# Performance work log

Hardware: AMD Instinct MI355X
Metric: run time of the kernel (lower is better)

Reference implementation:

```python
import jax, jax.numpy as jnp
import numpy as np

KERNEL_EPS = 1e-4  # performer-pytorch softmax_kernel eps


def _softmax_kernel(data, projection, is_query):
    # data: [b, h, n, d]; projection: [m, d]
    d = data.shape[-1]
    m = projection.shape[0]
    data_normalizer = d ** -0.25
    ratio = m ** -0.5
    # random-feature logits: [b, h, n, m]
    data_dash = jnp.einsum('bhnd,md->bhnm', data * data_normalizer, projection)
    # ||x||^2 / 2 * normalizer^2, [b, h, n, 1]
    diag = 0.5 * (data_normalizer ** 2) * jnp.sum(data * data, axis=-1, keepdims=True)
    if is_query:
        stab = jnp.max(data_dash, axis=-1, keepdims=True)
    else:
        stab = jnp.max(data_dash)  # global max, as in performer-pytorch
    return ratio * (jnp.exp(data_dash - diag - stab) + KERNEL_EPS)


def _linear_attention(q, k, v):
    # q, k: [b, h, n, m] random features; v: [b, h, n, e]
    k_cumsum = jnp.sum(k, axis=-2)                                   # [b, h, m]
    d_inv = 1.0 / jnp.einsum('bhnm,bhm->bhn', q, k_cumsum)           # [b, h, n]
    context = jnp.einsum('bhnm,bhne->bhme', k, v)                    # [b, h, m, e]
    return jnp.einsum('bhme,bhnm,bhn->bhne', context, q, d_inv)      # [b, h, n, e]


def setup_inputs() -> dict:
    key = jax.random.key(0)
    kq, kk, kv = jax.random.split(key, 3)
    b, h, n, d = 8, 16, 4096, 64
    nb_features = 256
    query = jax.random.normal(kq, (b, h, n, d), dtype=jnp.float32)
    key_t = jax.random.normal(kk, (b, h, n, d), dtype=jnp.float32)
    value = jax.random.normal(kv, (b, h, n, d), dtype=jnp.float32)
    # Gaussian orthogonal random matrix (performer-pytorch, scaling=0):
    # stack of d x d orthonormal blocks, rows rescaled to chi(d) norms.
    rng = np.random.RandomState(0)
    blocks = []
    for _ in range(nb_features // d + 1):
        qmat, _ = np.linalg.qr(rng.randn(d, d))
        blocks.append(qmat.T)
    proj = np.concatenate(blocks, axis=0)[:nb_features]
    multiplier = np.linalg.norm(rng.randn(nb_features, d), axis=1)
    projection = jnp.asarray(multiplier[:, None] * proj, dtype=jnp.float32)
    return {"query": query, "key": key_t, "value": value, "projection": projection}


def reference(query, key, value, projection):
    q_prime = _softmax_kernel(query, projection, is_query=True)   # [b,h,n,m]
    k_prime = _softmax_kernel(key, projection, is_query=False)    # [b,h,n,m]
    return _linear_attention(q_prime, k_prime, value)             # [b,h,n,e]
```

## Files before the change

kernel.cpp:

```cpp
#include <hip/hip_runtime.h>
#include <hip/hip_bf16.h>

typedef __attribute__((ext_vector_type(4))) float f32x4;
typedef __attribute__((ext_vector_type(8))) short short8;
typedef __attribute__((ext_vector_type(4))) unsigned short us4;
typedef __attribute__((ext_vector_type(4))) unsigned int u32x4;

#define BH_ 128
#define N_ 4096
#define LOG2E 1.4426950408889634f
#define NORML (0.35355339059327373f * LOG2E)
#define DIAGL (0.0625f * LOG2E)
#define EPSF 1e-4f

#if __has_builtin(__builtin_amdgcn_exp2f)
#define EXP2F(x) __builtin_amdgcn_exp2f(x)
#else
#define EXP2F(x) exp2f(x)
#endif

#define BARRIER_LGKM() asm volatile("s_waitcnt lgkmcnt(0)\ns_barrier" ::: "memory")

static __device__ __forceinline__ unsigned short f2bf(float f) {
  return __bfloat16_as_ushort(__float2bfloat16(f));
}
static __device__ __forceinline__ float bf2f(unsigned short s) {
  return __uint_as_float(((unsigned int)s) << 16);
}
static __device__ __forceinline__ us4 cvt4(f32x4 x) {
  us4 r;
  r[0] = f2bf(x[0]); r[1] = f2bf(x[1]); r[2] = f2bf(x[2]); r[3] = f2bf(x[3]);
  return r;
}
static __device__ __forceinline__ unsigned int pk2bf(float lo, float hi) {
  unsigned int r;
  asm("v_cvt_pk_bf16_f32 %0, %1, %2" : "=v"(r) : "v"(lo), "v"(hi));
  return r;
}

static __device__ __forceinline__ int posm(int m) {
  return (m & 0xE0) | ((m & 0xC) << 1) | ((m & 0x10) >> 2) | (m & 3);
}

__global__ void perf_prep(const float* __restrict__ proj,
                          unsigned short* __restrict__ projb) {
  int i = blockIdx.x * 256 + threadIdx.x;
  projb[i] = f2bf(proj[i] * NORML);
}

__global__ __launch_bounds__(256, 2)
void perf_kpass(const float* __restrict__ kp, const float* __restrict__ vp,
                const float* __restrict__ proj, float* __restrict__ ctxp,
                float* __restrict__ kexpp, float* __restrict__ vsump,
                unsigned int* __restrict__ gmaxb, int nchunk) {
  const int bh = blockIdx.x & (BH_ - 1);
  const int chunk = blockIdx.x >> 7;
  const int chunkrows = N_ / nchunk;
  const int tiles = chunkrows >> 5;
  const int t = threadIdx.x;
  const int wid = t >> 6;
  const int lane = t & 63;
  const int g = lane >> 4;
  const int c = lane & 15;

  __shared__ __align__(16) unsigned short sX[2][32][72];
  __shared__ __align__(16) unsigned short sVt[2][64][40];
  __shared__ float sDiag[2][32];
  __shared__ float sVsum[64];
  __shared__ float sGm[4];

  short8 pfrag[4][2];
#pragma unroll
  for (int mt = 0; mt < 4; ++mt)
#pragma unroll
    for (int kk = 0; kk < 2; ++kk) {
      const float* src = proj + (wid * 64 + mt * 16 + c) * 64 + kk * 32 + g * 8;
      short8 v;
#pragma unroll
      for (int j = 0; j < 8; ++j) v[j] = (short)f2bf(src[j] * NORML);
      pfrag[mt][kk] = v;
    }

  f32x4 ctx[4][4];
#pragma unroll
  for (int i = 0; i < 4; ++i)
#pragma unroll
    for (int j = 0; j < 4; ++j) ctx[i][j] = (f32x4){0.f, 0.f, 0.f, 0.f};

  float kexpreg[4] = {0.f, 0.f, 0.f, 0.f};
  float vsum0 = 0.f, vsum1 = 0.f, vsum2 = 0.f, vsum3 = 0.f;
  float gm = -1e30f;

  const float* kb0 = kp + ((size_t)bh * N_ + (size_t)chunk * chunkrows) * 64;
  const float* vb0 = vp + ((size_t)bh * N_ + (size_t)chunk * chunkrows) * 64;

  f32x4 kx[2], vx[2];
#pragma unroll
  for (int hh = 0; hh < 2; ++hh) {
    int f = t + hh * 256;
    kx[hh] = *(const f32x4*)(kb0 + (f >> 4) * 64 + (f & 15) * 4);
    vx[hh] = *(const f32x4*)(vb0 + (f >> 4) * 64 + (f & 15) * 4);
  }

  for (int nt = 0; nt < tiles; ++nt) {
    const int buf = nt & 1;
#pragma unroll
    for (int hh = 0; hh < 2; ++hh) {
      int f = t + hh * 256;
      int row = f >> 4;
      int c4 = f & 15;
      f32x4 x = kx[hh];
      float ss = x[0] * x[0] + x[1] * x[1] + x[2] * x[2] + x[3] * x[3];
      ss += __shfl_xor(ss, 1);
      ss += __shfl_xor(ss, 2);
      ss += __shfl_xor(ss, 4);
      ss += __shfl_xor(ss, 8);
      if (c4 == 0) sDiag[buf][row] = DIAGL * ss;
      *(us4*)&sX[buf][row][c4 * 4] = cvt4(x);
      f32x4 vv = vx[hh];
      vsum0 += vv[0]; vsum1 += vv[1]; vsum2 += vv[2]; vsum3 += vv[3];
      const int ks = ((row >> 2) & 3) * 8 + (row >> 4) * 4 + (row & 3);
#pragma unroll
      for (int jj = 0; jj < 4; ++jj) {
        int j = (jj + t) & 3;
        float val = (j == 0) ? vv[0] : (j == 1) ? vv[1] : (j == 2) ? vv[2] : vv[3];
        sVt[buf][c4 * 4 + j][ks] = f2bf(val);
      }
    }
    if (nt + 1 < tiles) {
      const float* kb = kb0 + (nt + 1) * 2048;
      const float* vb = vb0 + (nt + 1) * 2048;
#pragma unroll
      for (int hh = 0; hh < 2; ++hh) {
        int f = t + hh * 256;
        kx[hh] = *(const f32x4*)(kb + (f >> 4) * 64 + (f & 15) * 4);
        vx[hh] = *(const f32x4*)(vb + (f >> 4) * 64 + (f & 15) * 4);
      }
    }
    BARRIER_LGKM();

    short8 afr[2][2];
#pragma unroll
    for (int nh1 = 0; nh1 < 2; ++nh1)
#pragma unroll
      for (int kk = 0; kk < 2; ++kk)
        afr[nh1][kk] = *(const short8*)&sX[buf][nh1 * 16 + c][kk * 32 + g * 8];

    f32x4 acc1[2][4];
#pragma unroll
    for (int i = 0; i < 2; ++i)
#pragma unroll
      for (int j = 0; j < 4; ++j) acc1[i][j] = (f32x4){0.f, 0.f, 0.f, 0.f};
#pragma unroll
    for (int kk = 0; kk < 2; ++kk)
#pragma unroll
      for (int nh1 = 0; nh1 < 2; ++nh1)
#pragma unroll
        for (int mt = 0; mt < 4; ++mt)
          acc1[nh1][mt] = __builtin_amdgcn_mfma_f32_16x16x32_bf16(
              afr[nh1][kk], pfrag[mt][kk], acc1[nh1][mt], 0, 0, 0);

    short8 wfrag[4];
#pragma unroll
    for (int mt = 0; mt < 4; ++mt) {
#pragma unroll
      for (int nh1 = 0; nh1 < 2; ++nh1)
#pragma unroll
        for (int r = 0; r < 4; ++r) {
          float dd = acc1[nh1][mt][r];
          gm = fmaxf(gm, dd);
          int n = nh1 * 16 + g * 4 + r;
          float w = EXP2F(dd - sDiag[buf][n]);
          unsigned short wb = f2bf(w);
          kexpreg[mt] += bf2f(wb);
          wfrag[mt][nh1 * 4 + r] = (short)wb;
        }
    }

    short8 bvv[4];
#pragma unroll
    for (int et = 0; et < 4; ++et)
      bvv[et] = *(const short8*)&sVt[buf][et * 16 + c][g * 8];
#pragma unroll
    for (int mt2 = 0; mt2 < 4; ++mt2)
#pragma unroll
      for (int et = 0; et < 4; ++et)
        ctx[mt2][et] = __builtin_amdgcn_mfma_f32_16x16x32_bf16(
            wfrag[mt2], bvv[et], ctx[mt2][et], 0, 0, 0);
  }

#pragma unroll
  for (int mt2 = 0; mt2 < 4; ++mt2)
#pragma unroll
    for (int et = 0; et < 4; ++et) {
      int m0 = wid * 64 + mt2 * 16 + g * 4;
      int e = et * 16 + c;
      size_t base = (((size_t)chunk * BH_ + bh) * 64 + e) * 256 + m0;
      *(f32x4*)(ctxp + base) = ctx[mt2][et];
    }
#pragma unroll
  for (int mt = 0; mt < 4; ++mt) {
    float s = kexpreg[mt];
    s += __shfl_xor(s, 16);
    s += __shfl_xor(s, 32);
    if (lane < 16)
      kexpp[((size_t)chunk * BH_ + bh) * 256 + wid * 64 + mt * 16 + lane] = s;
  }
  if (t < 64) sVsum[t] = 0.f;
  __syncthreads();
  atomicAdd(&sVsum[(t & 15) * 4 + 0], vsum0);
  atomicAdd(&sVsum[(t & 15) * 4 + 1], vsum1);
  atomicAdd(&sVsum[(t & 15) * 4 + 2], vsum2);
  atomicAdd(&sVsum[(t & 15) * 4 + 3], vsum3);
  __syncthreads();
  if (t < 64) vsump[((size_t)chunk * BH_ + bh) * 64 + t] = sVsum[t];

  gm = fmaxf(gm, __shfl_xor(gm, 1));
  gm = fmaxf(gm, __shfl_xor(gm, 2));
  gm = fmaxf(gm, __shfl_xor(gm, 4));
  gm = fmaxf(gm, __shfl_xor(gm, 8));
  gm = fmaxf(gm, __shfl_xor(gm, 16));
  gm = fmaxf(gm, __shfl_xor(gm, 32));
  if (lane == 0) sGm[wid] = gm;
  __syncthreads();
  if (t == 0) {
    float mm = fmaxf(fmaxf(sGm[0], sGm[1]), fmaxf(sGm[2], sGm[3]));
    atomicMax((int*)gmaxb, __float_as_int(mm));
  }
}

__global__ void perf_rescale(const float* __restrict__ ctxp,
                             const float* __restrict__ kexpp,
                             const float* __restrict__ vsump,
                             unsigned short* __restrict__ ctxt,
                             unsigned short* __restrict__ kchi,
                             unsigned short* __restrict__ kclo,
                             const unsigned int* __restrict__ gmaxb, int nchunk) {
  const int bh = blockIdx.x >> 3;
  const int es = blockIdx.x & 7;
  const int t = threadIdx.x;
  const int pos = posm(t);
  const float gmax = __uint_as_float(*gmaxb);
  const float s = EXP2F(-gmax);
  if (es == 0) {
    float acc = 0.f;
    for (int cc = 0; cc < nchunk; ++cc)
      acc += kexpp[((size_t)cc * BH_ + bh) * 256 + t];
    float kcv = s * acc + EPSF * (float)N_;
    unsigned short hi = f2bf(kcv);
    kchi[bh * 256 + pos] = hi;
    kclo[bh * 256 + pos] = f2bf(kcv - bf2f(hi));
  }
  for (int e = es * 8; e < es * 8 + 8; ++e) {
    float vs = 0.f;
    for (int cc = 0; cc < nchunk; ++cc)
      vs += vsump[((size_t)cc * BH_ + bh) * 64 + e];
    float a2 = 0.f;
    for (int cc = 0; cc < nchunk; ++cc)
      a2 += ctxp[(((size_t)cc * BH_ + bh) * 64 + e) * 256 + t];
    ctxt[((size_t)bh * 64 + e) * 256 + pos] = f2bf(s * a2 + EPSF * vs);
  }
}

__global__ __launch_bounds__(256, 2)
void perf_qpass(const float* __restrict__ qp,
                const unsigned short* __restrict__ projb,
                const unsigned short* __restrict__ ctxt,
                const unsigned short* __restrict__ kchi,
                const unsigned short* __restrict__ kclo,
                float* __restrict__ outp) {
  const int bh = blockIdx.x >> 3;
  const int chunk = blockIdx.x & 7;
  const int t = threadIdx.x;
  const int wid = t >> 6;
  const int lane = t & 63;
  const int g = lane >> 4;
  const int c = lane & 15;

  __shared__ __align__(16) unsigned short sP[256 * 64];
  __shared__ __align__(16) unsigned short sC[64 * 256];
  __shared__ __align__(16) unsigned short sC2[16 * 256];

  const unsigned short* csrc = ctxt + (size_t)bh * 64 * 256;
  const unsigned short* khib = kchi + bh * 256;
  const unsigned short* klob = kclo + bh * 256;

  const float* qbase = qp + ((size_t)bh * N_ + chunk * 512 + wid * 128) * 64;
  float* obase = outp + ((size_t)bh * N_ + chunk * 512 + wid * 128) * 64;

  const float* q0 = qbase + (size_t)c * 64 + g * 8;
  f32x4 xp0 = *(const f32x4*)(q0);
  f32x4 xp1 = *(const f32x4*)(q0 + 4);
  f32x4 xp2 = *(const f32x4*)(q0 + 32);
  f32x4 xp3 = *(const f32x4*)(q0 + 36);

#pragma unroll
  for (int rep = 0; rep < 8; ++rep) {
    int e = rep * 2048 + t * 8;
    {
      int row = e >> 6, slot = (e & 63) >> 3;
      short8 v = *(const short8*)(projb + e);
      *(short8*)((char*)sP + row * 128 + ((slot ^ (row & 7)) << 4)) = v;
    }
    {
      int row = e >> 8, slot = (e & 255) >> 3;
      short8 v = *(const short8*)(csrc + e);
      *(short8*)((char*)sC + row * 512 + ((slot ^ (row & 7)) << 4)) = v;
    }
  }
#pragma unroll
  for (int rep = 0; rep < 2; ++rep) {
    int e = rep * 2048 + t * 8;
    int row = e >> 8, col = e & 255, slot = col >> 3;
    short8 v = {0, 0, 0, 0, 0, 0, 0, 0};
    if (row == 0) v = *(const short8*)(khib + col);
    if (row == 1) v = *(const short8*)(klob + col);
    *(short8*)((char*)sC2 + row * 512 + ((slot ^ (row & 7)) << 4)) = v;
  }
  __syncthreads();

  const int gsw = (g ^ (c & 3)) << 4;
  const int b6 = (c >> 2) & 1;
  const int pb0 = c * 128 + (b6 << 6) + gsw;
  const int pb1 = c * 128 + ((1 ^ b6) << 6) + gsw;
  const char* spc = (const char*)sP;
  const char* scc = (const char*)sC + c * 512;
  const char* sc2c = (const char*)sC2 + c * 512;

#pragma unroll 1
  for (int tt = 0; tt < 8; ++tt) {
    f32x4 x0 = xp0, x1 = xp1, x2 = xp2, x3 = xp3;
    if (tt + 1 < 8) {
      const float* qn = qbase + ((size_t)((tt + 1) * 16 + c)) * 64 + g * 8;
      xp0 = *(const f32x4*)(qn);
      xp1 = *(const f32x4*)(qn + 4);
      xp2 = *(const f32x4*)(qn + 32);
      xp3 = *(const f32x4*)(qn + 36);
    }
    float ss = x0[0]*x0[0] + x0[1]*x0[1] + x0[2]*x0[2] + x0[3]*x0[3]
             + x1[0]*x1[0] + x1[1]*x1[1] + x1[2]*x1[2] + x1[3]*x1[3]
             + x2[0]*x2[0] + x2[1]*x2[1] + x2[2]*x2[2] + x2[3]*x2[3]
             + x3[0]*x3[0] + x3[1]*x3[1] + x3[2]*x3[2] + x3[3]*x3[3];
    ss += __shfl_xor(ss, 16);
    ss += __shfl_xor(ss, 32);
    const float diag = DIAGL * ss;

    short8 xb0, xb1;
#pragma unroll
    for (int j = 0; j < 4; ++j) {
      xb0[j] = (short)f2bf(x0[j]);
      xb0[j + 4] = (short)f2bf(x1[j]);
      xb1[j] = (short)f2bf(x2[j]);
      xb1[j + 4] = (short)f2bf(x3[j]);
    }

    f32x4 acc1[16];
#pragma unroll
    for (int mt = 0; mt < 16; ++mt) acc1[mt] = (f32x4){0.f, 0.f, 0.f, 0.f};
    short8 Ak0[4], Ak1[4], Bk0[4], Bk1[4];
#pragma unroll
    for (int i = 0; i < 4; ++i) {
      Ak0[i] = *(const short8*)(spc + i * 2048 + pb0);
      Ak1[i] = *(const short8*)(spc + i * 2048 + pb1);
    }
#pragma unroll
    for (int i = 0; i < 4; ++i) {
      Bk0[i] = *(const short8*)(spc + (4 + i) * 2048 + pb0);
      Bk1[i] = *(const short8*)(spc + (4 + i) * 2048 + pb1);
    }
#pragma unroll
    for (int i = 0; i < 4; ++i) {
      acc1[i] = __builtin_amdgcn_mfma_f32_16x16x32_bf16(Ak0[i], xb0, acc1[i], 0, 0, 0);
      acc1[i] = __builtin_amdgcn_mfma_f32_16x16x32_bf16(Ak1[i], xb1, acc1[i], 0, 0, 0);
    }
#pragma unroll
    for (int i = 0; i < 4; ++i) {
      Ak0[i] = *(const short8*)(spc + (8 + i) * 2048 + pb0);
      Ak1[i] = *(const short8*)(spc + (8 + i) * 2048 + pb1);
    }
#pragma unroll
    for (int i = 0; i < 4; ++i) {
      acc1[4 + i] = __builtin_amdgcn_mfma_f32_16x16x32_bf16(Bk0[i], xb0, acc1[4 + i], 0, 0, 0);
      acc1[4 + i] = __builtin_amdgcn_mfma_f32_16x16x32_bf16(Bk1[i], xb1, acc1[4 + i], 0, 0, 0);
    }
#pragma unroll
    for (int i = 0; i < 4; ++i) {
      Bk0[i] = *(const short8*)(spc + (12 + i) * 2048 + pb0);
      Bk1[i] = *(const short8*)(spc + (12 + i) * 2048 + pb1);
    }
#pragma unroll
    for (int i = 0; i < 4; ++i) {
      acc1[8 + i] = __builtin_amdgcn_mfma_f32_16x16x32_bf16(Ak0[i], xb0, acc1[8 + i], 0, 0, 0);
      acc1[8 + i] = __builtin_amdgcn_mfma_f32_16x16x32_bf16(Ak1[i], xb1, acc1[8 + i], 0, 0, 0);
    }
#pragma unroll
    for (int i = 0; i < 4; ++i) {
      acc1[12 + i] = __builtin_amdgcn_mfma_f32_16x16x32_bf16(Bk0[i], xb0, acc1[12 + i], 0, 0, 0);
      acc1[12 + i] = __builtin_amdgcn_mfma_f32_16x16x32_bf16(Bk1[i], xb1, acc1[12 + i], 0, 0, 0);
    }

    float mx = acc1[0][0];
#pragma unroll
    for (int mt = 0; mt < 16; ++mt)
#pragma unroll
      for (int r = 0; r < 4; ++r) mx = fmaxf(mx, acc1[mt][r]);
    mx = fmaxf(mx, __shfl_xor(mx, 16));
    mx = fmaxf(mx, __shfl_xor(mx, 32));
    const float base = diag + mx;

    uint2 qtp[16];
#pragma unroll
    for (int mt = 0; mt < 16; ++mt) {
      float qa = EXP2F(acc1[mt][0] - base) + EPSF;
      float qb = EXP2F(acc1[mt][1] - base) + EPSF;
      float qc = EXP2F(acc1[mt][2] - base) + EPSF;
      float qd = EXP2F(acc1[mt][3] - base) + EPSF;
      qtp[mt].x = pk2bf(qa, qb);
      qtp[mt].y = pk2bf(qc, qd);
    }

    f32x4 acc2[5];
#pragma unroll
    for (int et = 0; et < 5; ++et) acc2[et] = (f32x4){0.f, 0.f, 0.f, 0.f};
#pragma unroll
    for (int w = 0; w < 8; ++w) {
      const int colb = ((w ^ b6) << 6) + gsw;
      short8 b0 = *(const short8*)(scc + colb);
      short8 b1 = *(const short8*)(scc + colb + 8192);
      short8 b2 = *(const short8*)(scc + colb + 16384);
      short8 b3 = *(const short8*)(scc + colb + 24576);
      short8 bd = *(const short8*)(sc2c + colb);
      u32x4 av = {qtp[2 * w].x, qtp[2 * w].y, qtp[2 * w + 1].x, qtp[2 * w + 1].y};
      short8 a = __builtin_bit_cast(short8, av);
      acc2[0] = __builtin_amdgcn_mfma_f32_16x16x32_bf16(a, b0, acc2[0], 0, 0, 0);
      acc2[1] = __builtin_amdgcn_mfma_f32_16x16x32_bf16(a, b1, acc2[1], 0, 0, 0);
      acc2[2] = __builtin_amdgcn_mfma_f32_16x16x32_bf16(a, b2, acc2[2], 0, 0, 0);
      acc2[3] = __builtin_amdgcn_mfma_f32_16x16x32_bf16(a, b3, acc2[3], 0, 0, 0);
      acc2[4] = __builtin_amdgcn_mfma_f32_16x16x32_bf16(a, bd, acc2[4], 0, 0, 0);
    }

    float* ot = obase + (size_t)tt * 16 * 64;
#pragma unroll
    for (int r = 0; r < 4; ++r) {
      float den = __shfl(acc2[4][r], g * 16) + __shfl(acc2[4][r], g * 16 + 1);
      float rinv = 1.0f / den;
      int n = g * 4 + r;
#pragma unroll
      for (int et = 0; et < 4; ++et)
        ot[(size_t)n * 64 + et * 16 + c] = acc2[et][r] * rinv;
    }
  }
}

extern "C" void kernel_launch(void* const* d_in, const int* in_sizes, int n_in,
                              void* d_out, int out_size, void* d_ws, size_t ws_size,
                              hipStream_t stream) {
  (void)in_sizes; (void)n_in; (void)out_size;
  const float* qp = (const float*)d_in[0];
  const float* kp = (const float*)d_in[1];
  const float* vp = (const float*)d_in[2];
  const float* proj = (const float*)d_in[3];
  float* outp = (float*)d_out;

  int nchunk = 8;
  while (nchunk > 1) {
    size_t fl = 64 + (size_t)nchunk * (2097152 + 32768 + 8192);
    size_t needed = fl * 4 + (size_t)(2097152 + 32768 + 32768 + 16384) * 2;
    if (needed <= ws_size) break;
    nchunk >>= 1;
  }

  float* wsf = (float*)d_ws;
  unsigned int* gmaxb = (unsigned int*)d_ws;
  float* ctxp = wsf + 64;
  float* kexpp = ctxp + (size_t)nchunk * 128 * 64 * 256;
  float* vsump = kexpp + (size_t)nchunk * 128 * 256;
  unsigned short* ctxt = (unsigned short*)(vsump + (size_t)nchunk * 128 * 64);
  unsigned short* kchi = ctxt + (size_t)128 * 64 * 256;
  unsigned short* kclo = kchi + 128 * 256;
  unsigned short* projb = kclo + 128 * 256;

  hipMemsetAsync(d_ws, 0, 16, stream);
  hipLaunchKernelGGL(perf_prep, dim3(64), dim3(256), 0, stream, proj, projb);
  hipLaunchKernelGGL(perf_kpass, dim3(128 * nchunk), dim3(256), 0, stream,
                     kp, vp, proj, ctxp, kexpp, vsump, gmaxb, nchunk);
  hipLaunchKernelGGL(perf_rescale, dim3(128 * 8), dim3(256), 0, stream,
                     ctxp, kexpp, vsump, ctxt, kchi, kclo, gmaxb, nchunk);
  hipLaunchKernelGGL(perf_qpass, dim3(128 * 8), dim3(256), 0, stream,
                     qp, projb, ctxt, kchi, kclo, outp);
}
```

Measured before the change: 201.0 us.

## Double K-pass tile rows and fold key-feature sums into MFMA with ones vector

The key pass now processes 64 rows per tile instead of 32. That halves the number of tile iterations and barriers, and each loaded projection fragment feeds twice the MFMA work. The per-feature sum of exponentials moves from scalar adds plus shuffles into an MFMA against a vector of bf16 ones. Conversions to bf16 now use packed v_cvt_pk_bf16_f32, and diag values are read as a vector. The change raises register and LDS use, which may reduce occupancy under launch_bounds(256,2).

```diff
diff --git a/kernel.cpp b/kernel.cpp
--- a/kernel.cpp
+++ b/kernel.cpp
@@ -27,15 +27,16 @@
 static __device__ __forceinline__ float bf2f(unsigned short s) {
   return __uint_as_float(((unsigned int)s) << 16);
 }
-static __device__ __forceinline__ us4 cvt4(f32x4 x) {
-  us4 r;
-  r[0] = f2bf(x[0]); r[1] = f2bf(x[1]); r[2] = f2bf(x[2]); r[3] = f2bf(x[3]);
-  return r;
-}
 static __device__ __forceinline__ unsigned int pk2bf(float lo, float hi) {
   unsigned int r;
   asm("v_cvt_pk_bf16_f32 %0, %1, %2" : "=v"(r) : "v"(lo), "v"(hi));
   return r;
+}
+static __device__ __forceinline__ us4 cvt4(f32x4 x) {
+  uint2 d;
+  d.x = pk2bf(x[0], x[1]);
+  d.y = pk2bf(x[2], x[3]);
+  return __builtin_bit_cast(us4, d);
 }
 
 static __device__ __forceinline__ int posm(int m) {
@@ -56,16 +57,16 @@
   const int bh = blockIdx.x & (BH_ - 1);
   const int chunk = blockIdx.x >> 7;
   const int chunkrows = N_ / nchunk;
-  const int tiles = chunkrows >> 5;
+  const int tiles = chunkrows >> 6;
   const int t = threadIdx.x;
   const int wid = t >> 6;
   const int lane = t & 63;
   const int g = lane >> 4;
   const int c = lane & 15;
 
-  __shared__ __align__(16) unsigned short sX[2][32][72];
-  __shared__ __align__(16) unsigned short sVt[2][64][40];
-  __shared__ float sDiag[2][32];
+  __shared__ __align__(16) unsigned short sX[2][64][72];
+  __shared__ __align__(16) unsigned short sVt[2][2][64][40];
+  __shared__ float sDiag[2][64];
   __shared__ float sVsum[64];
   __shared__ float sGm[4];
 
@@ -81,22 +82,28 @@
       pfrag[mt][kk] = v;
     }
 
+  short8 ones;
+#pragma unroll
+  for (int j = 0; j < 8; ++j) ones[j] = (short)0x3F80;
+
   f32x4 ctx[4][4];
 #pragma unroll
   for (int i = 0; i < 4; ++i)
 #pragma unroll
     for (int j = 0; j < 4; ++j) ctx[i][j] = (f32x4){0.f, 0.f, 0.f, 0.f};
-
-  float kexpreg[4] = {0.f, 0.f, 0.f, 0.f};
+  f32x4 kexpacc[4];
+#pragma unroll
+  for (int i = 0; i < 4; ++i) kexpacc[i] = (f32x4){0.f, 0.f, 0.f, 0.f};
+
   float vsum0 = 0.f, vsum1 = 0.f, vsum2 = 0.f, vsum3 = 0.f;
   float gm = -1e30f;
 
   const float* kb0 = kp + ((size_t)bh * N_ + (size_t)chunk * chunkrows) * 64;
   const float* vb0 = vp + ((size_t)bh * N_ + (size_t)chunk * chunkrows) * 64;
 
-  f32x4 kx[2], vx[2];
-#pragma unroll
-  for (int hh = 0; hh < 2; ++hh) {
+  f32x4 kx[4], vx[4];
+#pragma unroll
+  for (int hh = 0; hh < 4; ++hh) {
     int f = t + hh * 256;
     kx[hh] = *(const f32x4*)(kb0 + (f >> 4) * 64 + (f & 15) * 4);
     vx[hh] = *(const f32x4*)(vb0 + (f >> 4) * 64 + (f & 15) * 4);
@@ -105,7 +112,7 @@
   for (int nt = 0; nt < tiles; ++nt) {
     const int buf = nt & 1;
 #pragma unroll
-    for (int hh = 0; hh < 2; ++hh) {
+    for (int hh = 0; hh < 4; ++hh) {
       int f = t + hh * 256;
       int row = f >> 4;
       int c4 = f & 15;
@@ -119,19 +126,21 @@
       *(us4*)&sX[buf][row][c4 * 4] = cvt4(x);
       f32x4 vv = vx[hh];
       vsum0 += vv[0]; vsum1 += vv[1]; vsum2 += vv[2]; vsum3 += vv[3];
-      const int ks = ((row >> 2) & 3) * 8 + (row >> 4) * 4 + (row & 3);
+      const int nn = row & 31;
+      const int s = row >> 5;
+      const int ks = ((nn >> 2) & 3) * 8 + (nn >> 4) * 4 + (nn & 3);
 #pragma unroll
       for (int jj = 0; jj < 4; ++jj) {
         int j = (jj + t) & 3;
         float val = (j == 0) ? vv[0] : (j == 1) ? vv[1] : (j == 2) ? vv[2] : vv[3];
-        sVt[buf][c4 * 4 + j][ks] = f2bf(val);
+        sVt[buf][s][c4 * 4 + j][ks] = f2bf(val);
       }
     }
     if (nt + 1 < tiles) {
-      const float* kb = kb0 + (nt + 1) * 2048;
-      const float* vb = vb0 + (nt + 1) * 2048;
-#pragma unroll
-      for (int hh = 0; hh < 2; ++hh) {
+      const float* kb = kb0 + (nt + 1) * 4096;
+      const float* vb = vb0 + (nt + 1) * 4096;
+#pragma unroll
+      for (int hh = 0; hh < 4; ++hh) {
         int f = t + hh * 256;
         kx[hh] = *(const f32x4*)(kb + (f >> 4) * 64 + (f & 15) * 4);
         vx[hh] = *(const f32x4*)(vb + (f >> 4) * 64 + (f & 15) * 4);
@@ -139,54 +148,63 @@
     }
     BARRIER_LGKM();
 
-    short8 afr[2][2];
-#pragma unroll
-    for (int nh1 = 0; nh1 < 2; ++nh1)
+    short8 afr[4][2];
+#pragma unroll
+    for (int nh = 0; nh < 4; ++nh)
 #pragma unroll
       for (int kk = 0; kk < 2; ++kk)
-        afr[nh1][kk] = *(const short8*)&sX[buf][nh1 * 16 + c][kk * 32 + g * 8];
-
-    f32x4 acc1[2][4];
-#pragma unroll
-    for (int i = 0; i < 2; ++i)
+        afr[nh][kk] = *(const short8*)&sX[buf][nh * 16 + c][kk * 32 + g * 8];
+
+    f32x4 acc1[4][4];
+#pragma unroll
+    for (int i = 0; i < 4; ++i)
 #pragma unroll
       for (int j = 0; j < 4; ++j) acc1[i][j] = (f32x4){0.f, 0.f, 0.f, 0.f};
 #pragma unroll
     for (int kk = 0; kk < 2; ++kk)
 #pragma unroll
-      for (int nh1 = 0; nh1 < 2; ++nh1)
+      for (int nh = 0; nh < 4; ++nh)
 #pragma unroll
         for (int mt = 0; mt < 4; ++mt)
-          acc1[nh1][mt] = __builtin_amdgcn_mfma_f32_16x16x32_bf16(
-              afr[nh1][kk], pfrag[mt][kk], acc1[nh1][mt], 0, 0, 0);
-
-    short8 wfrag[4];
+          acc1[nh][mt] = __builtin_amdgcn_mfma_f32_16x16x32_bf16(
+              afr[nh][kk], pfrag[mt][kk], acc1[nh][mt], 0, 0, 0);
+
+    f32x4 dg[4];
+#pragma unroll
+    for (int nh = 0; nh < 4; ++nh)
+      dg[nh] = *(const f32x4*)&sDiag[buf][nh * 16 + g * 4];
+
+    short8 bvv[2][4];
+#pragma unroll
+    for (int s = 0; s < 2; ++s)
+#pragma unroll
+      for (int et = 0; et < 4; ++et)
+        bvv[s][et] = *(const short8*)&sVt[buf][s][et * 16 + c][g * 8];
+
 #pragma unroll
     for (int mt = 0; mt < 4; ++mt) {
-#pragma unroll
-      for (int nh1 = 0; nh1 < 2; ++nh1)
-#pragma unroll
-        for (int r = 0; r < 4; ++r) {
-          float dd = acc1[nh1][mt][r];
-          gm = fmaxf(gm, dd);
-          int n = nh1 * 16 + g * 4 + r;
-          float w = EXP2F(dd - sDiag[buf][n]);
-          unsigned short wb = f2bf(w);
-          kexpreg[mt] += bf2f(wb);
-          wfrag[mt][nh1 * 4 + r] = (short)wb;
-        }
-    }
-
-    short8 bvv[4];
-#pragma unroll
-    for (int et = 0; et < 4; ++et)
-      bvv[et] = *(const short8*)&sVt[buf][et * 16 + c][g * 8];
-#pragma unroll
-    for (int mt2 = 0; mt2 < 4; ++mt2)
-#pragma unroll
-      for (int et = 0; et < 4; ++et)
-        ctx[mt2][et] = __builtin_amdgcn_mfma_f32_16x16x32_bf16(
-            wfrag[mt2], bvv[et], ctx[mt2][et], 0, 0, 0);
+      unsigned int wd[8];
+#pragma unroll
+      for (int nh = 0; nh < 4; ++nh) {
+        f32x4 dd = acc1[nh][mt];
+        gm = fmaxf(gm, fmaxf(fmaxf(dd[0], dd[1]), fmaxf(dd[2], dd[3])));
+        float w0 = EXP2F(dd[0] - dg[nh][0]);
+        float w1 = EXP2F(dd[1] - dg[nh][1]);
+        float w2 = EXP2F(dd[2] - dg[nh][2]);
+        float w3 = EXP2F(dd[3] - dg[nh][3]);
+        wd[nh * 2] = pk2bf(w0, w1);
+        wd[nh * 2 + 1] = pk2bf(w2, w3);
+      }
+      short8 ws0 = __builtin_bit_cast(short8, (u32x4){wd[0], wd[1], wd[2], wd[3]});
+      short8 ws1 = __builtin_bit_cast(short8, (u32x4){wd[4], wd[5], wd[6], wd[7]});
+      kexpacc[mt] = __builtin_amdgcn_mfma_f32_16x16x32_bf16(ws0, ones, kexpacc[mt], 0, 0, 0);
+      kexpacc[mt] = __builtin_amdgcn_mfma_f32_16x16x32_bf16(ws1, ones, kexpacc[mt], 0, 0, 0);
+#pragma unroll
+      for (int et = 0; et < 4; ++et) {
+        ctx[mt][et] = __builtin_amdgcn_mfma_f32_16x16x32_bf16(ws0, bvv[0][et], ctx[mt][et], 0, 0, 0);
+        ctx[mt][et] = __builtin_amdgcn_mfma_f32_16x16x32_bf16(ws1, bvv[1][et], ctx[mt][et], 0, 0, 0);
+      }
+    }
   }
 
 #pragma unroll
@@ -198,13 +216,13 @@
       size_t base = (((size_t)chunk * BH_ + bh) * 64 + e) * 256 + m0;
       *(f32x4*)(ctxp + base) = ctx[mt2][et];
     }
-#pragma unroll
-  for (int mt = 0; mt < 4; ++mt) {
-    float s = kexpreg[mt];
-    s += __shfl_xor(s, 16);
-    s += __shfl_xor(s, 32);
-    if (lane < 16)
-      kexpp[((size_t)chunk * BH_ + bh) * 256 + wid * 64 + mt * 16 + lane] = s;
+  if (c == 0) {
+#pragma unroll
+    for (int mt = 0; mt < 4; ++mt)
+#pragma unroll
+      for (int r = 0; r < 4; ++r)
+        kexpp[((size_t)chunk * BH_ + bh) * 256 + wid * 64 + mt * 16 + g * 4 + r] =
+            kexpacc[mt][r];
   }
   if (t < 64) sVsum[t] = 0.f;
   __syncthreads();
```

After: 322.6 us. 60.5% more time.

## Load K fragments directly from global and stage V in 256-row phases

Applied to the files above, without the earlier changes.

The key-pass kernel no longer stages K through shared memory. Each wave reads its MFMA A-fragments straight from global memory and computes the row squared norms with cross-lane shuffles instead of a shared diag array. V is transposed into an 8-slot shared buffer covering 256 rows per phase, which cuts barriers from one per 32-row tile to two per phase. In exchange, each of the 4 waves reloads the same K tile from global (relying on cache), and the register prefetch is gone, so global-load latency is less hidden.

```diff
diff --git a/kernel.cpp b/kernel.cpp
--- a/kernel.cpp
+++ b/kernel.cpp
@@ -26,11 +26,6 @@
 }
 static __device__ __forceinline__ float bf2f(unsigned short s) {
   return __uint_as_float(((unsigned int)s) << 16);
-}
-static __device__ __forceinline__ us4 cvt4(f32x4 x) {
-  us4 r;
-  r[0] = f2bf(x[0]); r[1] = f2bf(x[1]); r[2] = f2bf(x[2]); r[3] = f2bf(x[3]);
-  return r;
 }
 static __device__ __forceinline__ unsigned int pk2bf(float lo, float hi) {
   unsigned int r;
@@ -56,16 +51,14 @@
   const int bh = blockIdx.x & (BH_ - 1);
   const int chunk = blockIdx.x >> 7;
   const int chunkrows = N_ / nchunk;
-  const int tiles = chunkrows >> 5;
+  const int phases = chunkrows >> 8;
   const int t = threadIdx.x;
   const int wid = t >> 6;
   const int lane = t & 63;
   const int g = lane >> 4;
   const int c = lane & 15;
 
-  __shared__ __align__(16) unsigned short sX[2][32][72];
-  __shared__ __align__(16) unsigned short sVt[2][64][40];
-  __shared__ float sDiag[2][32];
+  __shared__ __align__(16) unsigned short sVt[8][64][40];
   __shared__ float sVsum[64];
   __shared__ float sGm[4];
 
@@ -94,99 +87,107 @@
   const float* kb0 = kp + ((size_t)bh * N_ + (size_t)chunk * chunkrows) * 64;
   const float* vb0 = vp + ((size_t)bh * N_ + (size_t)chunk * chunkrows) * 64;
 
-  f32x4 kx[2], vx[2];
-#pragma unroll
-  for (int hh = 0; hh < 2; ++hh) {
-    int f = t + hh * 256;
-    kx[hh] = *(const f32x4*)(kb0 + (f >> 4) * 64 + (f & 15) * 4);
-    vx[hh] = *(const f32x4*)(vb0 + (f >> 4) * 64 + (f & 15) * 4);
-  }
-
-  for (int nt = 0; nt < tiles; ++nt) {
-    const int buf = nt & 1;
-#pragma unroll
-    for (int hh = 0; hh < 2; ++hh) {
-      int f = t + hh * 256;
-      int row = f >> 4;
+  for (int p = 0; p < phases; ++p) {
+    if (p) BARRIER_LGKM();
+
+#pragma unroll 4
+    for (int rep = 0; rep < 16; ++rep) {
+      int f = rep * 256 + t;
+      int rl = f >> 4;
       int c4 = f & 15;
-      f32x4 x = kx[hh];
-      float ss = x[0] * x[0] + x[1] * x[1] + x[2] * x[2] + x[3] * x[3];
-      ss += __shfl_xor(ss, 1);
-      ss += __shfl_xor(ss, 2);
-      ss += __shfl_xor(ss, 4);
-      ss += __shfl_xor(ss, 8);
-      if (c4 == 0) sDiag[buf][row] = DIAGL * ss;
-      *(us4*)&sX[buf][row][c4 * 4] = cvt4(x);
-      f32x4 vv = vx[hh];
+      f32x4 vv = *(const f32x4*)(vb0 + ((size_t)(p * 256 + rl)) * 64 + c4 * 4);
       vsum0 += vv[0]; vsum1 += vv[1]; vsum2 += vv[2]; vsum3 += vv[3];
-      const int ks = ((row >> 2) & 3) * 8 + (row >> 4) * 4 + (row & 3);
+      int ts8 = rl >> 5;
+      int n32 = rl & 31;
+      int ks = ((n32 >> 2) & 3) * 8 + (n32 >> 4) * 4 + (n32 & 3);
 #pragma unroll
       for (int jj = 0; jj < 4; ++jj) {
         int j = (jj + t) & 3;
         float val = (j == 0) ? vv[0] : (j == 1) ? vv[1] : (j == 2) ? vv[2] : vv[3];
-        sVt[buf][c4 * 4 + j][ks] = f2bf(val);
+        sVt[ts8][c4 * 4 + j][ks] = f2bf(val);
       }
     }
-    if (nt + 1 < tiles) {
-      const float* kb = kb0 + (nt + 1) * 2048;
-      const float* vb = vb0 + (nt + 1) * 2048;
-#pragma unroll
-      for (int hh = 0; hh < 2; ++hh) {
-        int f = t + hh * 256;
-        kx[hh] = *(const f32x4*)(kb + (f >> 4) * 64 + (f & 15) * 4);
-        vx[hh] = *(const f32x4*)(vb + (f >> 4) * 64 + (f & 15) * 4);
+    BARRIER_LGKM();
+
+#pragma unroll 1
+    for (int ts = 0; ts < 8; ++ts) {
+      const float* xt = kb0 + ((size_t)(p * 256 + ts * 32)) * 64;
+
+      short8 afr[2][2];
+      float dgq[2];
+#pragma unroll
+      for (int nh1 = 0; nh1 < 2; ++nh1) {
+        const float* rowp = xt + (nh1 * 16 + c) * 64;
+        f32x4 a0 = *(const f32x4*)(rowp + g * 8);
+        f32x4 a1 = *(const f32x4*)(rowp + g * 8 + 4);
+        f32x4 a2 = *(const f32x4*)(rowp + 32 + g * 8);
+        f32x4 a3 = *(const f32x4*)(rowp + 32 + g * 8 + 4);
+        float ss = a0[0]*a0[0] + a0[1]*a0[1] + a0[2]*a0[2] + a0[3]*a0[3]
+                 + a1[0]*a1[0] + a1[1]*a1[1] + a1[2]*a1[2] + a1[3]*a1[3]
+                 + a2[0]*a2[0] + a2[1]*a2[1] + a2[2]*a2[2] + a2[3]*a2[3]
+                 + a3[0]*a3[0] + a3[1]*a3[1] + a3[2]*a3[2] + a3[3]*a3[3];
+        ss += __shfl_xor(ss, 16);
+        ss += __shfl_xor(ss, 32);
+        dgq[nh1] = DIAGL * ss;
+        short8 v0, v1;
+#pragma unroll
+        for (int j = 0; j < 4; ++j) {
+          v0[j] = (short)f2bf(a0[j]);
+          v0[j + 4] = (short)f2bf(a1[j]);
+          v1[j] = (short)f2bf(a2[j]);
+          v1[j + 4] = (short)f2bf(a3[j]);
+        }
+        afr[nh1][0] = v0;
+        afr[nh1][1] = v1;
       }
-    }
-    BARRIER_LGKM();
-
-    short8 afr[2][2];
-#pragma unroll
-    for (int nh1 = 0; nh1 < 2; ++nh1)
+      float dgn[2][4];
+#pragma unroll
+      for (int nh1 = 0; nh1 < 2; ++nh1)
+#pragma unroll
+        for (int r = 0; r < 4; ++r)
+          dgn[nh1][r] = __shfl(dgq[nh1], g * 4 + r);
+
+      f32x4 acc1[2][4];
+#pragma unroll
+      for (int i = 0; i < 2; ++i)
+#pragma unroll
+        for (int j = 0; j < 4; ++j) acc1[i][j] = (f32x4){0.f, 0.f, 0.f, 0.f};
 #pragma unroll
       for (int kk = 0; kk < 2; ++kk)
-        afr[nh1][kk] = *(const short8*)&sX[buf][nh1 * 16 + c][kk * 32 + g * 8];
-
-    f32x4 acc1[2][4];
-#pragma unroll
-    for (int i = 0; i < 2; ++i)
-#pragma unroll
-      for (int j = 0; j < 4; ++j) acc1[i][j] = (f32x4){0.f, 0.f, 0.f, 0.f};
-#pragma unroll
-    for (int kk = 0; kk < 2; ++kk)
-#pragma unroll
-      for (int nh1 = 0; nh1 < 2; ++nh1)
-#pragma unroll
-        for (int mt = 0; mt < 4; ++mt)
-          acc1[nh1][mt] = __builtin_amdgcn_mfma_f32_16x16x32_bf16(
-              afr[nh1][kk], pfrag[mt][kk], acc1[nh1][mt], 0, 0, 0);
-
-    short8 wfrag[4];
-#pragma unroll
-    for (int mt = 0; mt < 4; ++mt) {
-#pragma unroll
-      for (int nh1 = 0; nh1 < 2; ++nh1)
-#pragma unroll
-        for (int r = 0; r < 4; ++r) {
-          float dd = acc1[nh1][mt][r];
-          gm = fmaxf(gm, dd);
-          int n = nh1 * 16 + g * 4 + r;
-          float w = EXP2F(dd - sDiag[buf][n]);
-          unsigned short wb = f2bf(w);
-          kexpreg[mt] += bf2f(wb);
-          wfrag[mt][nh1 * 4 + r] = (short)wb;
-        }
-    }
-
-    short8 bvv[4];
-#pragma unroll
-    for (int et = 0; et < 4; ++et)
-      bvv[et] = *(const short8*)&sVt[buf][et * 16 + c][g * 8];
-#pragma unroll
-    for (int mt2 = 0; mt2 < 4; ++mt2)
+#pragma unroll
+        for (int nh1 = 0; nh1 < 2; ++nh1)
+#pragma unroll
+          for (int mt = 0; mt < 4; ++mt)
+            acc1[nh1][mt] = __builtin_amdgcn_mfma_f32_16x16x32_bf16(
+                afr[nh1][kk], pfrag[mt][kk], acc1[nh1][mt], 0, 0, 0);
+
+      short8 wfrag[4];
+#pragma unroll
+      for (int mt = 0; mt < 4; ++mt) {
+#pragma unroll
+        for (int nh1 = 0; nh1 < 2; ++nh1)
+#pragma unroll
+          for (int r = 0; r < 4; ++r) {
+            float dd = acc1[nh1][mt][r];
+            gm = fmaxf(gm, dd);
+            float w = EXP2F(dd - dgn[nh1][r]);
+            unsigned short wb = f2bf(w);
+            kexpreg[mt] += bf2f(wb);
+            wfrag[mt][nh1 * 4 + r] = (short)wb;
+          }
+      }
+
+      short8 bvv[4];
 #pragma unroll
       for (int et = 0; et < 4; ++et)
-        ctx[mt2][et] = __builtin_amdgcn_mfma_f32_16x16x32_bf16(
-            wfrag[mt2], bvv[et], ctx[mt2][et], 0, 0, 0);
+        bvv[et] = *(const short8*)&sVt[ts][et * 16 + c][g * 8];
+#pragma unroll
+      for (int mt2 = 0; mt2 < 4; ++mt2)
+#pragma unroll
+        for (int et = 0; et < 4; ++et)
+          ctx[mt2][et] = __builtin_amdgcn_mfma_f32_16x16x32_bf16(
+              wfrag[mt2], bvv[et], ctx[mt2][et], 0, 0, 0);
+    }
   }
 
 #pragma unroll
```

Measured after the change: 249.7 us. +24.2%, slower.
